# Kernel optimization log

Measured on AMD Instinct MI355X. Metric: run time of the kernel, lower is better.

The kernel has to match this reference:

```python
import jax, jax.numpy as jnp
import numpy as np

BATCH, SEQ, IN, HID = 8192, 512, 5, 64


def setup_inputs() -> dict:
    key = jax.random.key(0)
    ks = jax.random.split(key, 7)
    s_ih = 1.0 / np.sqrt(HID)
    return {
        "inputs": jax.random.normal(ks[0], (BATCH, SEQ, IN), dtype=jnp.float32),
        "W_ih": jax.random.uniform(ks[1], (4 * HID, IN), minval=-s_ih, maxval=s_ih, dtype=jnp.float32),
        "W_hh": jax.random.uniform(ks[2], (4 * HID, HID), minval=-s_ih, maxval=s_ih, dtype=jnp.float32),
        "b_ih": jax.random.uniform(ks[3], (4 * HID,), minval=-s_ih, maxval=s_ih, dtype=jnp.float32),
        "b_hh": jax.random.uniform(ks[4], (4 * HID,), minval=-s_ih, maxval=s_ih, dtype=jnp.float32),
        "fc_w": jax.random.uniform(ks[5], (1, HID), minval=-s_ih, maxval=s_ih, dtype=jnp.float32),
        "fc_b": jax.random.uniform(ks[6], (1,), minval=-s_ih, maxval=s_ih, dtype=jnp.float32),
    }


def reference(inputs, W_ih, W_hh, b_ih, b_hh, fc_w, fc_b):
    B = inputs.shape[0]
    # Precompute input projections for all timesteps: [S, B, 4H]
    x_proj = jnp.einsum('bsi,gi->sbg', inputs, W_ih) + b_ih + b_hh

    def step(carry, xg):
        hx, cx = carry
        gates = xg + hx @ W_hh.T  # [B, 4H]
        i, f, g, o = jnp.split(gates, 4, axis=-1)  # PyTorch LSTMCell gate order
        i = jax.nn.sigmoid(i)
        f = jax.nn.sigmoid(f)
        g = jnp.tanh(g)
        o = jax.nn.sigmoid(o)
        cx = f * cx + i * g
        hx = o * jnp.tanh(cx)
        return (hx, cx), None

    h0 = jnp.zeros((B, HID), dtype=inputs.dtype)
    c0 = jnp.zeros((B, HID), dtype=inputs.dtype)
    (hx, _), _ = jax.lax.scan(step, (h0, c0), x_proj)
    pred = hx @ fc_w.T + fc_b  # [B, 1]
    return jax.nn.leaky_relu(pred, negative_slope=0.01)
```

## Files before the change

### kernel.cpp

```cpp
#include <hip/hip_runtime.h>

#define BATCH 8192
#define SEQ 512
#define INND 5
#define HID 64

typedef __attribute__((ext_vector_type(8))) short short8;
typedef __attribute__((ext_vector_type(4))) float f32x4;

__device__ __forceinline__ unsigned short f2bf(float f) {
  union { float f; unsigned u; } v; v.f = f;
  unsigned r = v.u + 0x7FFFu + ((v.u >> 16) & 1u);
  return (unsigned short)(r >> 16);
}
__device__ __forceinline__ float bf2f(unsigned short s) {
  union { unsigned u; float f; } v; v.u = ((unsigned)s) << 16;
  return v.f;
}
__device__ __forceinline__ float sigm(float z) {
  return __builtin_amdgcn_rcpf(1.f + __expf(-z));
}
__device__ __forceinline__ float tanh_(float z) {
  return 1.f - 2.f * __builtin_amdgcn_rcpf(1.f + __expf(2.f * z));
}

__global__ __launch_bounds__(256) void lstm_kernel(
    const float* __restrict__ inputs, const float* __restrict__ W_ih,
    const float* __restrict__ W_hh, const float* __restrict__ b_ih,
    const float* __restrict__ b_hh, const float* __restrict__ fc_w,
    const float* __restrict__ fc_b, float* __restrict__ out) {
  __shared__ unsigned short hbuf[2][16][104] __attribute__((aligned(16)));

  const int tid = threadIdx.x;
  const int lane = tid & 63;
  const int w = tid >> 6;
  const int l15 = lane & 15;
  const int kg = lane >> 4;
  const int b0 = blockIdx.x * 16;

  short8 wf[4][3];
#pragma unroll
  for (int X = 0; X < 4; ++X) {
    const int col = 64 * X + 16 * w + l15;
    const float* wr = W_hh + col * 64;
#pragma unroll
    for (int s = 0; s < 2; ++s) {
      const float* p = wr + 32 * s + 8 * kg;
      short8 v;
#pragma unroll
      for (int j = 0; j < 8; ++j) v[j] = (short)f2bf(p[j]);
      wf[X][s] = v;
    }
    short8 e;
#pragma unroll
    for (int j = 0; j < 8; ++j) e[j] = 0;
    if (kg == 0) {
#pragma unroll
      for (int j = 0; j < 5; ++j) e[j] = (short)f2bf(W_ih[col * 5 + j]);
      e[5] = (short)f2bf(b_ih[col] + b_hh[col]);
    }
    wf[X][2] = e;
  }

  const bool writer = (tid < 16 * INND);
  const int wrow = tid / INND;
  const int wi = tid - wrow * INND;
  const float* xptr = inputs + (size_t)(b0 + wrow) * (SEQ * INND) + wi;

  for (int i = tid; i < 2 * 16 * 104; i += 256) ((unsigned short*)hbuf)[i] = 0;
  __syncthreads();
  if (tid < 32) hbuf[tid >> 4][tid & 15][69] = 0x3F80;
  float x_next = 0.f;
  if (writer) {
    hbuf[0][wrow][64 + wi] = f2bf(xptr[0]);
    x_next = xptr[INND];
  }
  __syncthreads();

  float cst[4] = {0.f, 0.f, 0.f, 0.f};
  for (int t = 0; t < SEQ; ++t) {
    const int cur = t & 1, nxt = cur ^ 1;

    float x_n2 = 0.f;
    if (writer && t + 2 < SEQ) x_n2 = xptr[(t + 2) * INND];

    f32x4 acc0 = {0.f, 0.f, 0.f, 0.f};
    f32x4 acc1 = {0.f, 0.f, 0.f, 0.f};
    f32x4 acc2 = {0.f, 0.f, 0.f, 0.f};
    f32x4 acc3 = {0.f, 0.f, 0.f, 0.f};
#pragma unroll
    for (int s = 0; s < 3; ++s) {
      const short8 a = *(const short8*)&hbuf[cur][l15][s * 32 + kg * 8];
      acc0 = __builtin_amdgcn_mfma_f32_16x16x32_bf16(a, wf[0][s], acc0, 0, 0, 0);
      acc1 = __builtin_amdgcn_mfma_f32_16x16x32_bf16(a, wf[1][s], acc1, 0, 0, 0);
      acc2 = __builtin_amdgcn_mfma_f32_16x16x32_bf16(a, wf[2][s], acc2, 0, 0, 0);
      ac3:;
      acc3 = __builtin_amdgcn_mfma_f32_16x16x32_bf16(a, wf[3][s], acc3, 0, 0, 0);
    }

    unsigned short hw[4];
#pragma unroll
    for (int q = 0; q < 4; ++q) {
      const float iz = sigm(acc0[q]);
      const float fz = sigm(acc1[q]);
      const float gz = tanh_(acc2[q]);
      const float oz = sigm(acc3[q]);
      const float cq = fz * cst[q] + iz * gz;
      cst[q] = cq;
      hw[q] = f2bf(oz * tanh_(cq));
    }
#pragma unroll
    for (int q = 0; q < 4; ++q)
      hbuf[nxt][kg * 4 + q][w * 16 + l15] = hw[q];
    if (writer && t + 1 < SEQ) hbuf[nxt][wrow][64 + wi] = f2bf(x_next);
    x_next = x_n2;
    __syncthreads();
  }

  if (tid < 64) {
    const int row = tid >> 2, seg = tid & 3;
    float sum = 0.f;
#pragma unroll
    for (int j = 0; j < 16; ++j)
      sum += bf2f(hbuf[0][row][seg * 16 + j]) * fc_w[seg * 16 + j];
    sum += __shfl_xor(sum, 1);
    sum += __shfl_xor(sum, 2);
    if (seg == 0) {
      const float p = sum + fc_b[0];
      out[b0 + row] = p > 0.f ? p : 0.01f * p;
    }
  }
}

extern "C" void kernel_launch(void* const* d_in, const int* in_sizes, int n_in,
                              void* d_out, int out_size, void* d_ws, size_t ws_size,
                              hipStream_t stream) {
  const float* inputs = (const float*)d_in[0];
  const float* W_ih = (const float*)d_in[1];
  const float* W_hh = (const float*)d_in[2];
  const float* b_ih = (const float*)d_in[3];
  const float* b_hh = (const float*)d_in[4];
  const float* fc_w = (const float*)d_in[5];
  const float* fc_b = (const float*)d_in[6];
  float* out = (float*)d_out;

  lstm_kernel<<<BATCH / 16, 256, 0, stream>>>(inputs, W_ih, W_hh, b_ih, b_hh,
                                              fc_w, fc_b, out);
}
```

Baseline: 513.7 us.

## Transpose MFMA operands, swizzle LDS layout, and share reciprocals across gate activations

Swaps the MFMA operand order so each lane gets 4 consecutive hidden units of one batch row, which allows packed 8-byte h stores into an XOR-swizzled LDS layout meant to avoid bank conflicts. Pre-scales the weights by -1 (and -2 for the g gate) so the activations become exp(z) directly. The i, f, g, o gates are then computed from one shared reciprocal of the product of their denominators, using packed float2 math. This cuts transcendental and rcp work per step, at the cost of clamps to prevent overflow and some extra rounding error.

```diff
diff --git a/kernel.cpp b/kernel.cpp
--- a/kernel.cpp
+++ b/kernel.cpp
@@ -4,9 +4,11 @@
 #define SEQ 512
 #define INND 5
 #define HID 64
+#define STRIDE 104
 
 typedef __attribute__((ext_vector_type(8))) short short8;
 typedef __attribute__((ext_vector_type(4))) float f32x4;
+typedef __attribute__((ext_vector_type(2))) float f32x2;
 
 __device__ __forceinline__ unsigned short f2bf(float f) {
   union { float f; unsigned u; } v; v.f = f;
@@ -17,30 +19,27 @@
   union { unsigned u; float f; } v; v.u = ((unsigned)s) << 16;
   return v.f;
 }
-__device__ __forceinline__ float sigm(float z) {
-  return __builtin_amdgcn_rcpf(1.f + __expf(-z));
-}
-__device__ __forceinline__ float tanh_(float z) {
-  return 1.f - 2.f * __builtin_amdgcn_rcpf(1.f + __expf(2.f * z));
-}
+#define RCP(x) __builtin_amdgcn_rcpf(x)
 
 __global__ __launch_bounds__(256) void lstm_kernel(
     const float* __restrict__ inputs, const float* __restrict__ W_ih,
     const float* __restrict__ W_hh, const float* __restrict__ b_ih,
     const float* __restrict__ b_hh, const float* __restrict__ fc_w,
     const float* __restrict__ fc_b, float* __restrict__ out) {
-  __shared__ unsigned short hbuf[2][16][104] __attribute__((aligned(16)));
+  __shared__ unsigned short hbuf[2][16][STRIDE] __attribute__((aligned(16)));
 
   const int tid = threadIdx.x;
   const int lane = tid & 63;
   const int w = tid >> 6;
   const int l15 = lane & 15;
   const int kg = lane >> 4;
+  const int l7 = l15 & 7;
   const int b0 = blockIdx.x * 16;
 
   short8 wf[4][3];
 #pragma unroll
   for (int X = 0; X < 4; ++X) {
+    const float sc = (X == 2) ? -2.f : -1.f;
     const int col = 64 * X + 16 * w + l15;
     const float* wr = W_hh + col * 64;
 #pragma unroll
@@ -48,7 +47,7 @@
       const float* p = wr + 32 * s + 8 * kg;
       short8 v;
 #pragma unroll
-      for (int j = 0; j < 8; ++j) v[j] = (short)f2bf(p[j]);
+      for (int j = 0; j < 8; ++j) v[j] = (short)f2bf(sc * p[j]);
       wf[X][s] = v;
     }
     short8 e;
@@ -56,73 +55,119 @@
     for (int j = 0; j < 8; ++j) e[j] = 0;
     if (kg == 0) {
 #pragma unroll
-      for (int j = 0; j < 5; ++j) e[j] = (short)f2bf(W_ih[col * 5 + j]);
-      e[5] = (short)f2bf(b_ih[col] + b_hh[col]);
+      for (int j = 0; j < 5; ++j) e[j] = (short)f2bf(sc * W_ih[col * 5 + j]);
+      e[5] = (short)f2bf(sc * (b_ih[col] + b_hh[col]));
     }
     wf[X][2] = e;
   }
+
+  unsigned short* const hb0 = &hbuf[0][0][0];
+  const int rd0 = l15 * STRIDE + ((kg ^ l7) << 3);
+  const int rd1 = l15 * STRIDE + (((4 | kg) ^ l7) << 3);
+  const int rd2 = l15 * STRIDE + 64 + ((kg ^ (l15 & 3)) << 3);
+  const int hwr = l15 * STRIDE + (((w << 4) | (kg << 2)) ^ (l7 << 3));
 
   const bool writer = (tid < 16 * INND);
   const int wrow = tid / INND;
   const int wi = tid - wrow * INND;
   const float* xptr = inputs + (size_t)(b0 + wrow) * (SEQ * INND) + wi;
+  const int xcol = 64 + (wi | ((wrow & 3) << 3));
 
-  for (int i = tid; i < 2 * 16 * 104; i += 256) ((unsigned short*)hbuf)[i] = 0;
+  for (int i = tid; i < 2 * 16 * STRIDE; i += 256) hb0[i] = 0;
   __syncthreads();
-  if (tid < 32) hbuf[tid >> 4][tid & 15][69] = 0x3F80;
+  if (tid < 32) {
+    const int r = tid & 15;
+    hbuf[tid >> 4][r][64 + (5 | ((r & 3) << 3))] = 0x3F80;
+  }
   float x_next = 0.f;
   if (writer) {
-    hbuf[0][wrow][64 + wi] = f2bf(xptr[0]);
+    hbuf[0][wrow][xcol] = f2bf(xptr[0]);
     x_next = xptr[INND];
   }
   __syncthreads();
 
-  float cst[4] = {0.f, 0.f, 0.f, 0.f};
+  f32x2 cst[2] = {{0.f, 0.f}, {0.f, 0.f}};
   for (int t = 0; t < SEQ; ++t) {
     const int cur = t & 1, nxt = cur ^ 1;
 
     float x_n2 = 0.f;
     if (writer && t + 2 < SEQ) x_n2 = xptr[(t + 2) * INND];
 
+    const unsigned short* hc = hb0 + cur * (16 * STRIDE);
     f32x4 acc0 = {0.f, 0.f, 0.f, 0.f};
     f32x4 acc1 = {0.f, 0.f, 0.f, 0.f};
     f32x4 acc2 = {0.f, 0.f, 0.f, 0.f};
     f32x4 acc3 = {0.f, 0.f, 0.f, 0.f};
-#pragma unroll
-    for (int s = 0; s < 3; ++s) {
-      const short8 a = *(const short8*)&hbuf[cur][l15][s * 32 + kg * 8];
-      acc0 = __builtin_amdgcn_mfma_f32_16x16x32_bf16(a, wf[0][s], acc0, 0, 0, 0);
-      acc1 = __builtin_amdgcn_mfma_f32_16x16x32_bf16(a, wf[1][s], acc1, 0, 0, 0);
-      acc2 = __builtin_amdgcn_mfma_f32_16x16x32_bf16(a, wf[2][s], acc2, 0, 0, 0);
-      ac3:;
-      acc3 = __builtin_amdgcn_mfma_f32_16x16x32_bf16(a, wf[3][s], acc3, 0, 0, 0);
+    {
+      const short8 a0 = *(const short8*)(hc + rd0);
+      acc0 = __builtin_amdgcn_mfma_f32_16x16x32_bf16(wf[0][0], a0, acc0, 0, 0, 0);
+      acc1 = __builtin_amdgcn_mfma_f32_16x16x32_bf16(wf[1][0], a0, acc1, 0, 0, 0);
+      acc2 = __builtin_amdgcn_mfma_f32_16x16x32_bf16(wf[2][0], a0, acc2, 0, 0, 0);
+      acc3 = __builtin_amdgcn_mfma_f32_16x16x32_bf16(wf[3][0], a0, acc3, 0, 0, 0);
+      const short8 a1 = *(const short8*)(hc + rd1);
+      acc0 = __builtin_amdgcn_mfma_f32_16x16x32_bf16(wf[0][1], a1, acc0, 0, 0, 0);
+      acc1 = __builtin_amdgcn_mfma_f32_16x16x32_bf16(wf[1][1], a1, acc1, 0, 0, 0);
+      acc2 = __builtin_amdgcn_mfma_f32_16x16x32_bf16(wf[2][1], a1, acc2, 0, 0, 0);
+      acc3 = __builtin_amdgcn_mfma_f32_16x16x32_bf16(wf[3][1], a1, acc3, 0, 0, 0);
+      const short8 a2 = *(const short8*)(hc + rd2);
+      acc0 = __builtin_amdgcn_mfma_f32_16x16x32_bf16(wf[0][2], a2, acc0, 0, 0, 0);
+      acc1 = __builtin_amdgcn_mfma_f32_16x16x32_bf16(wf[1][2], a2, acc1, 0, 0, 0);
+      acc2 = __builtin_amdgcn_mfma_f32_16x16x32_bf16(wf[2][2], a2, acc2, 0, 0, 0);
+      acc3 = __builtin_amdgcn_mfma_f32_16x16x32_bf16(wf[3][2], a2, acc3, 0, 0, 0);
     }
 
-    unsigned short hw[4];
+    unsigned pk[2];
 #pragma unroll
-    for (int q = 0; q < 4; ++q) {
-      const float iz = sigm(acc0[q]);
-      const float fz = sigm(acc1[q]);
-      const float gz = tanh_(acc2[q]);
-      const float oz = sigm(acc3[q]);
-      const float cq = fz * cst[q] + iz * gz;
-      cst[q] = cq;
-      hw[q] = f2bf(oz * tanh_(cq));
+    for (int p = 0; p < 2; ++p) {
+      f32x2 ti = {acc0[2 * p], acc0[2 * p + 1]};
+      f32x2 tf = {acc1[2 * p], acc1[2 * p + 1]};
+      f32x2 tg = {acc2[2 * p], acc2[2 * p + 1]};
+      f32x2 to = {acc3[2 * p], acc3[2 * p + 1]};
+      ti.x = fminf(ti.x, 17.f); ti.y = fminf(ti.y, 17.f);
+      tf.x = fminf(tf.x, 17.f); tf.y = fminf(tf.y, 17.f);
+      tg.x = fminf(tg.x, 34.f); tg.y = fminf(tg.y, 34.f);
+      to.x = fminf(to.x, 17.f); to.y = fminf(to.y, 17.f);
+      f32x2 Ei, Ef, Eg, Eo;
+      Ei.x = __expf(ti.x); Ei.y = __expf(ti.y);
+      Ef.x = __expf(tf.x); Ef.y = __expf(tf.y);
+      Eg.x = __expf(tg.x); Eg.y = __expf(tg.y);
+      Eo.x = __expf(to.x); Eo.y = __expf(to.y);
+      const f32x2 ai = Ei + 1.f, af = Ef + 1.f, ag = Eg + 1.f, ao = Eo + 1.f;
+      const f32x2 u = ai * ag, v = af * ao;
+      const f32x2 P = u * v;
+      f32x2 r; r.x = RCP(P.x); r.y = RCP(P.y);
+      const f32x2 rv = r * v;
+      const f32x2 ru = r * u;
+      const f32x2 Pig = (1.f - Eg) * rv;
+      const f32x2 sf = ru * ao;
+      const f32x2 so = ru * af;
+      const f32x2 c = sf * cst[p] + Pig;
+      cst[p] = c;
+      f32x2 tc;
+      tc.x = fminf(-2.f * c.x, 80.f); tc.y = fminf(-2.f * c.y, 80.f);
+      f32x2 Ec; Ec.x = __expf(tc.x); Ec.y = __expf(tc.y);
+      const f32x2 ac = Ec + 1.f;
+      f32x2 rc; rc.x = RCP(ac.x); rc.y = RCP(ac.y);
+      const f32x2 th = (1.f - Ec) * rc;
+      const f32x2 h = so * th;
+      pk[p] = ((unsigned)f2bf(h.x)) | (((unsigned)f2bf(h.y)) << 16);
     }
-#pragma unroll
-    for (int q = 0; q < 4; ++q)
-      hbuf[nxt][kg * 4 + q][w * 16 + l15] = hw[q];
-    if (writer && t + 1 < SEQ) hbuf[nxt][wrow][64 + wi] = f2bf(x_next);
+    {
+      uint2 pkv; pkv.x = pk[0]; pkv.y = pk[1];
+      *(uint2*)(hb0 + nxt * (16 * STRIDE) + hwr) = pkv;
+    }
+    if (writer && t + 1 < SEQ) hbuf[nxt][wrow][xcol] = f2bf(x_next);
     x_next = x_n2;
     __syncthreads();
   }
 
   if (tid < 64) {
     const int row = tid >> 2, seg = tid & 3;
+    const int key = (row & 7) << 3;
     float sum = 0.f;
 #pragma unroll
     for (int j = 0; j < 16; ++j)
-      sum += bf2f(hbuf[0][row][seg * 16 + j]) * fc_w[seg * 16 + j];
+      sum += bf2f(hbuf[0][row][(seg * 16 + j) ^ key]) * fc_w[seg * 16 + j];
     sum += __shfl_xor(sum, 1);
     sum += __shfl_xor(sum, 2);
     if (seg == 0) {
```

Result: slower. 559.3 us (+8.9%).
